# Optimization experiments

Measured on AMD Instinct MI355X. Metric: run time of the kernel, lower is better.

The kernel has to match this reference:

```python
import jax, jax.numpy as jnp
from jax import lax
import numpy as np


def setup_inputs() -> dict:
    key = jax.random.key(0)
    kb, ks = jax.random.split(key)
    boxes = jax.random.uniform(kb, (4, 2048, 4), dtype=jnp.float32)
    scores = jax.random.normal(ks, (4, 16, 2048), dtype=jnp.float32)
    return {
        "boxes": boxes,
        "scores": scores,
        "max_output_boxes_per_class": 100,
        "iou_threshold": jnp.float32(0.5),
        "score_threshold": jnp.float32(0.0),
    }


def _fix_boxes(boxes):
    # center_point_box == 0 path: reorder corners so x1<=x2, y1<=y2
    # (swap-if-greater in the original is equivalent to per-axis min/max)
    x1, y1, x2, y2 = boxes[..., 0], boxes[..., 1], boxes[..., 2], boxes[..., 3]
    return jnp.stack(
        [jnp.minimum(x1, x2), jnp.minimum(y1, y2), jnp.maximum(x1, x2), jnp.maximum(y1, y2)],
        axis=-1,
    )


def _nms_single(boxes, scores, iou_thr, score_thr, K):
    # boxes: [N,4] (xyxy, already fixed), scores: [N]
    N = boxes.shape[0]
    order = jnp.argsort(-scores)  # stable sort -> ties broken by index, like torchvision
    b = boxes[order]
    x1, y1, x2, y2 = b[:, 0], b[:, 1], b[:, 2], b[:, 3]
    area = (x2 - x1) * (y2 - y1)
    idxs = jnp.arange(N)

    def step(suppressed, k):
        kept = ~suppressed[k]
        ix1 = jnp.maximum(b[k, 0], x1)
        iy1 = jnp.maximum(b[k, 1], y1)
        ix2 = jnp.minimum(b[k, 2], x2)
        iy2 = jnp.minimum(b[k, 3], y2)
        inter = jnp.maximum(ix2 - ix1, 0.0) * jnp.maximum(iy2 - iy1, 0.0)
        iou = inter / (area[k] + area - inter)
        suppressed = suppressed | (kept & (iou > iou_thr) & (idxs > k))
        return suppressed, kept

    _, keep = lax.scan(step, jnp.zeros((N,), bool), idxs)  # keep: [N] in score order
    rank = jnp.cumsum(keep) - 1
    slot = jnp.where(keep & (rank < K), rank, K)  # slot K is out-of-bounds -> dropped
    sel = jnp.full((K,), -1, jnp.int32).at[slot].set(order.astype(jnp.int32), mode="drop")
    # original truncates the top-K selection to the COUNT of selected boxes passing score_thr
    sel_valid = sel >= 0
    count = jnp.sum(sel_valid & (scores[jnp.maximum(sel, 0)] >= score_thr))
    return jnp.where(jnp.arange(K) < count, sel, -1)


def reference(boxes, scores, max_output_boxes_per_class, iou_threshold, score_threshold):
    B, N, _ = boxes.shape
    C = scores.shape[1]
    K = int(max_output_boxes_per_class)
    fb = _fix_boxes(boxes)
    f = lambda bx, sc: _nms_single(bx, sc, iou_threshold, score_threshold, K)
    # vmap over classes (boxes shared), then over batch
    sel = jax.vmap(jax.vmap(f, in_axes=(None, 0)), in_axes=(0, 0))(fb, scores)  # [B,C,K]
    valid = sel >= 0
    bidx = jnp.broadcast_to(jnp.arange(B, dtype=jnp.int32)[:, None, None], sel.shape)
    cidx = jnp.broadcast_to(jnp.arange(C, dtype=jnp.int32)[None, :, None], sel.shape)
    out = jnp.stack([jnp.where(valid, bidx, -1), jnp.where(valid, cidx, -1), sel], axis=-1)
    # fixed-shape padded version of the original ragged [num_selected, 3] output;
    # invalid rows are all -1
    return out.reshape(B * C * K, 3)
```

## Files before the change

### kernel.cpp

```cpp
#include <hip/hip_runtime.h>

#define NN 2048
#define NT 256
#define NE 8
#define NB 4
#define NC 16
#define NCLS (NB * NC)
#define TILE 64
#define NTILES (NN / TILE)
#define KKEEP 176

typedef unsigned long long u64;

__device__ __forceinline__ u64 make_key(float s, int idx) {
  unsigned u = __float_as_uint(s);
  u ^= (u >> 31) ? 0xFFFFFFFFu : 0x80000000u;
  u = ~u;
  return ((u64)u << 32) | (unsigned)idx;
}
__device__ __forceinline__ float key_score(u64 key) {
  unsigned u = ~(unsigned)(key >> 32);
  unsigned bits = (u >> 31) ? (u ^ 0x80000000u) : ~u;
  return __uint_as_float(bits);
}

__device__ __forceinline__ u64 shfl_xor_u64(u64 v, int h) {
  int lo = __shfl_xor((int)(unsigned)v, h, 64);
  int hi = __shfl_xor((int)(unsigned)(v >> 32), h, 64);
  return ((u64)(unsigned)hi << 32) | (unsigned)lo;
}

__device__ __forceinline__ float iou_f(float kx1, float ky1, float kx2, float ky2, float ka,
                                       float x1, float y1, float x2, float y2, float a) {
  float ix1 = fmaxf(kx1, x1);
  float iy1 = fmaxf(ky1, y1);
  float ix2 = fminf(kx2, x2);
  float iy2 = fminf(ky2, y2);
  float iw = fmaxf(ix2 - ix1, 0.0f);
  float ih = fmaxf(iy2 - iy1, 0.0f);
  float inter = iw * ih;
  asm volatile("" : "+v"(inter));
  float denom = ka + a - inter;
  return inter / denom;
}

__global__ __launch_bounds__(NT) void sort_kernel(
    const float* __restrict__ boxes,
    const float* __restrict__ scores,
    float* __restrict__ wx1, float* __restrict__ wy1,
    float* __restrict__ wx2, float* __restrict__ wy2,
    float* __restrict__ wsc, int* __restrict__ widx)
{
  __shared__ u64 s_key[NN];

  const int bc = blockIdx.x;
  const int b  = bc >> 4;
  const int t  = threadIdx.x;
  const int gbase = t * NE;

  u64 key[NE];
  {
    const float4* s4 = (const float4*)(scores + (size_t)bc * NN);
    float4 v0 = s4[t * 2], v1 = s4[t * 2 + 1];
    key[0] = make_key(v0.x, gbase + 0);
    key[1] = make_key(v0.y, gbase + 1);
    key[2] = make_key(v0.z, gbase + 2);
    key[3] = make_key(v0.w, gbase + 3);
    key[4] = make_key(v1.x, gbase + 4);
    key[5] = make_key(v1.y, gbase + 5);
    key[6] = make_key(v1.z, gbase + 6);
    key[7] = make_key(v1.w, gbase + 7);
  }

  for (int s = 2; s <= NN; s <<= 1) {
    for (int d = s >> 1; d > 0; d >>= 1) {
      if (d >= 512) {
        __syncthreads();
        for (int k = 0; k < NE; k++) s_key[gbase + k] = key[k];
        __syncthreads();
        const int pb = (t ^ (d >> 3)) * NE;
        const bool asc   = ((gbase & s) == 0);
        const bool lower = ((gbase & d) == 0);
        for (int k = 0; k < NE; k++) {
          u64 o = s_key[pb + k];
          bool take = (asc == lower) ? (o < key[k]) : (o > key[k]);
          if (take) key[k] = o;
        }
      } else if (d >= 8) {
        const int h = d >> 3;
        const bool asc   = ((gbase & s) == 0);
        const bool lower = ((t & h) == 0);
        for (int k = 0; k < NE; k++) {
          u64 o = shfl_xor_u64(key[k], h);
          bool take = (asc == lower) ? (o < key[k]) : (o > key[k]);
          if (take) key[k] = o;
        }
      } else {
        for (int k = 0; k < NE; k++) {
          int kk = k ^ d;
          if (kk > k) {
            bool asc = (((gbase + k) & s) == 0);
            bool sw  = asc ? (key[k] > key[kk]) : (key[k] < key[kk]);
            if (sw) { u64 tmp = key[k]; key[k] = key[kk]; key[kk] = tmp; }
          }
        }
      }
    }
  }

  const float* bbase = boxes + (size_t)b * NN * 4;
  const size_t obase = (size_t)bc * NN;
  for (int k = 0; k < NE; k++) {
    int g = gbase + k;
    int idx = (int)(unsigned)(key[k] & 0xFFFFFFFFu);
    float4 v = *(const float4*)(bbase + (size_t)idx * 4);
    float x1 = fminf(v.x, v.z), x2 = fmaxf(v.x, v.z);
    float y1 = fminf(v.y, v.w), y2 = fmaxf(v.y, v.w);
    wx1[obase + g] = x1; wy1[obase + g] = y1;
    wx2[obase + g] = x2; wy2[obase + g] = y2;
    wsc[obase + g] = key_score(key[k]);
    widx[obase + g] = idx;
  }
}

__global__ __launch_bounds__(NT) void greedy_kernel(
    const float* __restrict__ wx1, const float* __restrict__ wy1,
    const float* __restrict__ wx2, const float* __restrict__ wy2,
    const float* __restrict__ wsc, const int* __restrict__ widx,
    const float* __restrict__ iou_thr_p, const float* __restrict__ score_thr_p,
    int K, int* __restrict__ out)
{
  __shared__ float s_kx1[KKEEP], s_ky1[KKEEP], s_kx2[KKEEP], s_ky2[KKEEP], s_ka[KKEEP];
  __shared__ float s_tx1[TILE], s_ty1[TILE], s_tx2[TILE], s_ty2[TILE], s_ts[TILE];
  __shared__ int   s_tidx[TILE];
  __shared__ u64   s_colmask[4][TILE];
  __shared__ u64   s_dead[4];
  __shared__ int   s_total;

  const int bc = blockIdx.x;
  const int b  = bc >> 4;
  const int c  = bc & 15;
  const int t  = threadIdx.x;
  const int wv = t >> 6;
  const int ln = t & 63;

  const float iou_thr = *iou_thr_p;
  const float sthr    = *score_thr_p;

  int* orow = out + (size_t)bc * K * 3;
  for (int i = t; i < K * 3; i += NT) orow[i] = -1;
  if (t == 0) s_total = 0;

  const size_t base0 = (size_t)bc * NN;
  __syncthreads();

  for (int tile = 0; tile < NTILES; tile++) {
    const int base = tile * TILE;

    if      (wv == 0) { s_tx1[ln] = wx1[base0 + base + ln]; s_ts[ln]   = wsc[base0 + base + ln]; }
    else if (wv == 1) { s_ty1[ln] = wy1[base0 + base + ln]; s_tidx[ln] = widx[base0 + base + ln]; }
    else if (wv == 2) { s_tx2[ln] = wx2[base0 + base + ln]; }
    else              { s_ty2[ln] = wy2[base0 + base + ln]; }
    const int kcount = s_total;
    __syncthreads();

    float jx1 = s_tx1[ln], jy1 = s_ty1[ln], jx2 = s_tx2[ln], jy2 = s_ty2[ln];
    float ja  = (jx2 - jx1) * (jy2 - jy1);
    u64 m = 0ULL;
    for (int r = 0; r < 16; r++) {
      int il = wv * 16 + r;
      if (il < ln) {
        float rx1 = s_tx1[il], ry1 = s_ty1[il], rx2 = s_tx2[il], ry2 = s_ty2[il];
        float ra  = (rx2 - rx1) * (ry2 - ry1);
        float iou = iou_f(rx1, ry1, rx2, ry2, ra, jx1, jy1, jx2, jy2, ja);
        if (iou > iou_thr) m |= (1ULL << il);
      }
    }
    s_colmask[wv][ln] = m;

    bool dead = false;
    for (int ki = wv; ki < kcount; ki += 4) {
      float iou = iou_f(s_kx1[ki], s_ky1[ki], s_kx2[ki], s_ky2[ki], s_ka[ki],
                        jx1, jy1, jx2, jy2, ja);
      if (iou > iou_thr) { dead = true; break; }
    }
    s_dead[wv] = __ballot(dead);
    __syncthreads();

    if (t < 64) {
      u64 mc = s_colmask[0][ln] | s_colmask[1][ln] | s_colmask[2][ln] | s_colmask[3][ln];
      u64 alive = ~(s_dead[0] | s_dead[1] | s_dead[2] | s_dead[3]);
      for (int i = 0; i < TILE; i++) {
        if ((alive >> i) & 1ULL) {
          u64 kill = __ballot((int)((mc >> i) & 1ULL));
          alive &= ~kill;
        }
      }
      int total0 = s_total;
      bool kept = (alive >> ln) & 1ULL;
      int pos = __popcll(alive & ((1ULL << ln) - 1ULL));
      if (kept) {
        int kpos = total0 + pos;
        s_kx1[kpos] = jx1; s_ky1[kpos] = jy1;
        s_kx2[kpos] = jx2; s_ky2[kpos] = jy2; s_ka[kpos] = ja;
        if (kpos < K && s_ts[ln] >= sthr) {
          orow[kpos * 3 + 0] = b;
          orow[kpos * 3 + 1] = c;
          orow[kpos * 3 + 2] = s_tidx[ln];
        }
      }
      if (ln == 0) s_total = total0 + (int)__popcll(alive);
    }
    __syncthreads();
    if (s_total >= K) break;
  }
}

extern "C" void kernel_launch(void* const* d_in, const int* in_sizes, int n_in,
                              void* d_out, int out_size, void* d_ws, size_t ws_size,
                              hipStream_t stream) {
  const float* boxes  = (const float*)d_in[0];
  const float* scores = (const float*)d_in[1];
  const float* iou_p  = (const float*)d_in[3];
  const float* sth_p  = (const float*)d_in[4];
  int* out = (int*)d_out;

  const int K = out_size / (NCLS * 3);
  const size_t plane = (size_t)NCLS * NN;

  float* w   = (float*)d_ws;
  float* wx1 = w + 0 * plane;
  float* wy1 = w + 1 * plane;
  float* wx2 = w + 2 * plane;
  float* wy2 = w + 3 * plane;
  float* wsc = w + 4 * plane;
  int*  widx = (int*)(w + 5 * plane);

  hipLaunchKernelGGL(sort_kernel, dim3(NCLS), dim3(NT), 0, stream,
                     boxes, scores, wx1, wy1, wx2, wy2, wsc, widx);
  hipLaunchKernelGGL(greedy_kernel, dim3(NCLS), dim3(NT), 0, stream,
                     wx1, wy1, wx2, wy2, wsc, widx, iou_p, sth_p, K, out);
}
```

Before: 66.06 us.

## Replace bitonic sort with rank-by-counting spread across more blocks

Replaces the per-class bitonic sort (64 blocks, many shuffle and shared-memory stages) with a counting rank sort. Each class is split over 8 blocks, each thread computes its element's rank by comparing against all 2048 keys in LDS, and writes the result directly to its sorted position. This trades O(N log^2 N) work with many barriers for O(N^2) comparisons, exposing 512 blocks to fill more CUs. Each block reloads the full score row, and the LDS broadcast reads of the comparisons become the main cost.

```diff
diff --git a/kernel.cpp b/kernel.cpp
--- a/kernel.cpp
+++ b/kernel.cpp
@@ -2,10 +2,10 @@
 
 #define NN 2048
 #define NT 256
-#define NE 8
 #define NB 4
 #define NC 16
 #define NCLS (NB * NC)
+#define CHUNKS 8
 #define TILE 64
 #define NTILES (NN / TILE)
 #define KKEEP 176
@@ -22,12 +22,6 @@
   unsigned u = ~(unsigned)(key >> 32);
   unsigned bits = (u >> 31) ? (u ^ 0x80000000u) : ~u;
   return __uint_as_float(bits);
-}
-
-__device__ __forceinline__ u64 shfl_xor_u64(u64 v, int h) {
-  int lo = __shfl_xor((int)(unsigned)v, h, 64);
-  int hi = __shfl_xor((int)(unsigned)(v >> 32), h, 64);
-  return ((u64)(unsigned)hi << 32) | (unsigned)lo;
 }
 
 __device__ __forceinline__ float iou_f(float kx1, float ky1, float kx2, float ky2, float ka,
@@ -44,7 +38,7 @@
   return inter / denom;
 }
 
-__global__ __launch_bounds__(NT) void sort_kernel(
+__global__ __launch_bounds__(NT) void rank_kernel(
     const float* __restrict__ boxes,
     const float* __restrict__ scores,
     float* __restrict__ wx1, float* __restrict__ wy1,
@@ -53,74 +47,50 @@
 {
   __shared__ u64 s_key[NN];
 
-  const int bc = blockIdx.x;
-  const int b  = bc >> 4;
-  const int t  = threadIdx.x;
-  const int gbase = t * NE;
-
-  u64 key[NE];
+  const int blk   = blockIdx.x;
+  const int bc    = blk >> 3;
+  const int chunk = blk & 7;
+  const int b     = bc >> 4;
+  const int t     = threadIdx.x;
+
   {
     const float4* s4 = (const float4*)(scores + (size_t)bc * NN);
     float4 v0 = s4[t * 2], v1 = s4[t * 2 + 1];
-    key[0] = make_key(v0.x, gbase + 0);
-    key[1] = make_key(v0.y, gbase + 1);
-    key[2] = make_key(v0.z, gbase + 2);
-    key[3] = make_key(v0.w, gbase + 3);
-    key[4] = make_key(v1.x, gbase + 4);
-    key[5] = make_key(v1.y, gbase + 5);
-    key[6] = make_key(v1.z, gbase + 6);
-    key[7] = make_key(v1.w, gbase + 7);
+    const int g = t * 8;
+    s_key[g + 0] = make_key(v0.x, g + 0);
+    s_key[g + 1] = make_key(v0.y, g + 1);
+    s_key[g + 2] = make_key(v0.z, g + 2);
+    s_key[g + 3] = make_key(v0.w, g + 3);
+    s_key[g + 4] = make_key(v1.x, g + 4);
+    s_key[g + 5] = make_key(v1.y, g + 5);
+    s_key[g + 6] = make_key(v1.z, g + 6);
+    s_key[g + 7] = make_key(v1.w, g + 7);
   }
-
-  for (int s = 2; s <= NN; s <<= 1) {
-    for (int d = s >> 1; d > 0; d >>= 1) {
-      if (d >= 512) {
-        __syncthreads();
-        for (int k = 0; k < NE; k++) s_key[gbase + k] = key[k];
-        __syncthreads();
-        const int pb = (t ^ (d >> 3)) * NE;
-        const bool asc   = ((gbase & s) == 0);
-        const bool lower = ((gbase & d) == 0);
-        for (int k = 0; k < NE; k++) {
-          u64 o = s_key[pb + k];
-          bool take = (asc == lower) ? (o < key[k]) : (o > key[k]);
-          if (take) key[k] = o;
-        }
-      } else if (d >= 8) {
-        const int h = d >> 3;
-        const bool asc   = ((gbase & s) == 0);
-        const bool lower = ((t & h) == 0);
-        for (int k = 0; k < NE; k++) {
-          u64 o = shfl_xor_u64(key[k], h);
-          bool take = (asc == lower) ? (o < key[k]) : (o > key[k]);
-          if (take) key[k] = o;
-        }
-      } else {
-        for (int k = 0; k < NE; k++) {
-          int kk = k ^ d;
-          if (kk > k) {
-            bool asc = (((gbase + k) & s) == 0);
-            bool sw  = asc ? (key[k] > key[kk]) : (key[k] < key[kk]);
-            if (sw) { u64 tmp = key[k]; key[k] = key[kk]; key[kk] = tmp; }
-          }
-        }
-      }
-    }
+  __syncthreads();
+
+  const int i = chunk * NT + t;
+  const u64 my = s_key[i];
+
+  int r0 = 0, r1 = 0, r2 = 0, r3 = 0;
+#pragma unroll 4
+  for (int j = 0; j < NN; j += 4) {
+    r0 += (s_key[j + 0] < my) ? 1 : 0;
+    r1 += (s_key[j + 1] < my) ? 1 : 0;
+    r2 += (s_key[j + 2] < my) ? 1 : 0;
+    r3 += (s_key[j + 3] < my) ? 1 : 0;
   }
-
-  const float* bbase = boxes + (size_t)b * NN * 4;
-  const size_t obase = (size_t)bc * NN;
-  for (int k = 0; k < NE; k++) {
-    int g = gbase + k;
-    int idx = (int)(unsigned)(key[k] & 0xFFFFFFFFu);
-    float4 v = *(const float4*)(bbase + (size_t)idx * 4);
-    float x1 = fminf(v.x, v.z), x2 = fmaxf(v.x, v.z);
-    float y1 = fminf(v.y, v.w), y2 = fmaxf(v.y, v.w);
-    wx1[obase + g] = x1; wy1[obase + g] = y1;
-    wx2[obase + g] = x2; wy2[obase + g] = y2;
-    wsc[obase + g] = key_score(key[k]);
-    widx[obase + g] = idx;
-  }
+  const int rank = r0 + r1 + r2 + r3;
+
+  const int idx = (int)(unsigned)(my & 0xFFFFFFFFu);
+  float4 v = *(const float4*)(boxes + ((size_t)b * NN + idx) * 4);
+  float x1 = fminf(v.x, v.z), x2 = fmaxf(v.x, v.z);
+  float y1 = fminf(v.y, v.w), y2 = fmaxf(v.y, v.w);
+
+  const size_t o = (size_t)bc * NN + rank;
+  wx1[o] = x1; wy1[o] = y1;
+  wx2[o] = x2; wy2[o] = y2;
+  wsc[o] = key_score(my);
+  widx[o] = idx;
 }
 
 __global__ __launch_bounds__(NT) void greedy_kernel(
@@ -236,7 +206,7 @@
   float* wsc = w + 4 * plane;
   int*  widx = (int*)(w + 5 * plane);
 
-  hipLaunchKernelGGL(sort_kernel, dim3(NCLS), dim3(NT), 0, stream,
+  hipLaunchKernelGGL(rank_kernel, dim3(NCLS * CHUNKS), dim3(NT), 0, stream,
                      boxes, scores, wx1, wy1, wx2, wy2, wsc, widx);
   hipLaunchKernelGGL(greedy_kernel, dim3(NCLS), dim3(NT), 0, stream,
                      wx1, wy1, wx2, wy2, wsc, widx, iou_p, sth_p, K, out);
```

Measured after the change: 53.17 us. -19.5%, faster.
